# Performance work log

Measured on AMD Instinct MI355X. Metric: run time of the kernel, lower is better.

Reference implementation:

```python
import jax, jax.numpy as jnp
import numpy as np

H = 256
H2 = H // 2
N = 1024
T = 12
B = 4


def setup_inputs() -> dict:
    key = jax.random.key(0)
    ks = jax.random.split(key, 12)
    s = lambda fan_in: 1.0 / np.sqrt(fan_in)
    inp = {
        "node_embeddings": jax.random.normal(ks[0], (B, N, H), jnp.float32),
        # origin encoder: Linear(H,H) -> ReLU -> Linear(H,H2)
        "W1o": jax.random.normal(ks[1], (H, H), jnp.float32) * s(H),
        "b1o": jnp.zeros((H,), jnp.float32),
        "W2o": jax.random.normal(ks[2], (H, H2), jnp.float32) * s(H),
        "b2o": jnp.zeros((H2,), jnp.float32),
        # dest encoder
        "W1d": jax.random.normal(ks[3], (H, H), jnp.float32) * s(H),
        "b1d": jnp.zeros((H,), jnp.float32),
        "W2d": jax.random.normal(ks[4], (H, H2), jnp.float32) * s(H),
        "b2d": jnp.zeros((H2,), jnp.float32),
        # bilinear: out = o @ Wb @ d^T + bb  (torch nn.Bilinear(H2,H2,1))
        "Wb": jax.random.normal(ks[5], (H2, H2), jnp.float32) * s(H2),
        "bb": jnp.zeros((), jnp.float32),
        # horizon predictor: Linear(1, T) -> ReLU
        "wh": jax.random.normal(ks[6], (T,), jnp.float32),
        "bh": jnp.zeros((T,), jnp.float32),
    }
    return inp


def reference(node_embeddings, W1o, b1o, W2o, b2o, W1d, b1d, W2d, b2d, Wb, bb, wh, bh):
    # encoders (dropout is identity at eval)
    o = jax.nn.relu(node_embeddings @ W1o + b1o) @ W2o + b2o      # (B,N,H2)
    d = jax.nn.relu(node_embeddings @ W1d + b1d) @ W2d + b2d      # (B,N,H2)
    # bilinear score without materializing (B,N,N,H2):
    oW = jnp.einsum("bik,kl->bil", o, Wb)                          # (B,N,H2)
    scores = jnp.einsum("bil,bjl->bij", oW, d) + bb                # (B,N,N)
    # horizon predictor Linear(1,T)+ReLU, then permute to (B,T,N,N)
    pred = jax.nn.relu(scores[..., None] * wh + bh)                # (B,N,N,T)
    pred = jnp.transpose(pred, (0, 3, 1, 2))                       # (B,T,N,N)
    return jax.nn.relu(pred)
```

## Files before the change

kernel.cpp:

```cpp
#include <hip/hip_runtime.h>
#include <hip/hip_bf16.h>

constexpr int H  = 256;
constexpr int H2 = 128;
constexpr int N  = 1024;
constexpr int T  = 12;
constexpr int B  = 4;
constexpr int M  = B * N;

using short8 = __attribute__((ext_vector_type(8))) short;
using f32x4  = __attribute__((ext_vector_type(4))) float;

__device__ __forceinline__ unsigned short f2bf(float f) {
    union { float f; unsigned int u; } v; v.f = f;
    unsigned int u = v.u;
    u += 0x7FFFu + ((u >> 16) & 1u);
    return (unsigned short)(u >> 16);
}

__global__ void fold_wb_kernel(const float* __restrict__ W2o,
                               const float* __restrict__ b2o,
                               const float* __restrict__ Wb,
                               float* __restrict__ W2of,
                               float* __restrict__ b2of) {
    __shared__ float row[H2];
    const int i = blockIdx.x;
    const int j = threadIdx.x;
    const float* src = (i < H) ? (W2o + i * H2) : b2o;
    row[j] = src[j];
    __syncthreads();
    float acc = 0.f;
#pragma unroll 8
    for (int k = 0; k < H2; ++k) acc = fmaf(row[k], Wb[k * H2 + j], acc);
    if (i < H) W2of[i * H2 + j] = acc;
    else       b2of[j] = acc;
}

__global__ void prep_kernel(const float* __restrict__ x,
                            const float* __restrict__ W1o, const float* __restrict__ W1d,
                            const float* __restrict__ b1o, const float* __restrict__ b1d,
                            const float* __restrict__ W2of, const float* __restrict__ b2of,
                            const float* __restrict__ W2d,  const float* __restrict__ b2d,
                            unsigned short* __restrict__ xb,
                            unsigned short* __restrict__ W1T,
                            unsigned short* __restrict__ W2T,
                            float* __restrict__ bias1, float* __restrict__ bias2)
{
    const int NX  = M * H;
    const int NW1 = 512 * H;
    const int NW2 = 256 * H;
    const int TOT = NX + NW1 + NW2 + 512 + 256;
    for (int i = blockIdx.x * blockDim.x + threadIdx.x; i < TOT;
         i += gridDim.x * blockDim.x) {
        if (i < NX) {
            xb[i] = f2bf(x[i]);
        } else if (i < NX + NW1) {
            const int j = i - NX, n = j >> 8, k = j & 255;
            const float v = (n < 256) ? W1o[k * H + n] : W1d[k * H + (n - 256)];
            W1T[j] = f2bf(v);
        } else if (i < NX + NW1 + NW2) {
            const int j = i - NX - NW1, n = j >> 8, k = j & 255;
            const float v = (n < 128) ? W2of[k * H2 + n] : W2d[k * H2 + (n - 128)];
            W2T[j] = f2bf(v);
        } else if (i < NX + NW1 + NW2 + 512) {
            const int j = i - NX - NW1 - NW2;
            bias1[j] = (j < 256) ? b1o[j] : b1d[j - 256];
        } else {
            const int j = i - NX - NW1 - NW2 - 512;
            bias2[j] = (j < 128) ? b2of[j] : b2d[j - 128];
        }
    }
}

template<bool RELU>
__device__ __forceinline__ void enc_body(
    const unsigned short* __restrict__ A, int lda,
    const unsigned short* __restrict__ Bt,
    const float* __restrict__ bias,
    unsigned short* __restrict__ C, int ldc)
{
    __shared__ unsigned short Abuf[64 * 40];
    __shared__ unsigned short Bbuf[64 * 40];
    const int tid = threadIdx.x;
    const int w  = tid >> 6;
    const int l  = tid & 63;
    const int lr = tid >> 2;
    const int lk = (tid & 3) * 8;

    uint4 aR = *(const uint4*)(A + (size_t)lr * lda + lk);
    uint4 bR = *(const uint4*)(Bt + (size_t)lr * 256 + lk);

    f32x4 z = {0.f, 0.f, 0.f, 0.f};
    f32x4 acc[4] = {z, z, z, z};

    for (int kc = 0; kc < 256; kc += 32) {
        if (kc) __syncthreads();
        *(uint4*)&Abuf[lr * 40 + lk] = aR;
        *(uint4*)&Bbuf[lr * 40 + lk] = bR;
        __syncthreads();
        if (kc + 32 < 256) {
            aR = *(const uint4*)(A + (size_t)lr * lda + kc + 32 + lk);
            bR = *(const uint4*)(Bt + (size_t)lr * 256 + kc + 32 + lk);
        }
        const int q8 = (l >> 4) * 8;
        const short8 bf = *(const short8*)&Bbuf[(w * 16 + (l & 15)) * 40 + q8];
#pragma unroll
        for (int it = 0; it < 4; ++it) {
            const short8 af = *(const short8*)&Abuf[(it * 16 + (l & 15)) * 40 + q8];
            acc[it] = __builtin_amdgcn_mfma_f32_16x16x32_bf16(af, bf, acc[it], 0, 0, 0);
        }
    }

    const int n  = w * 16 + (l & 15);
    const int r0 = (l >> 4) * 4;
    const float bn = bias[n];
#pragma unroll
    for (int it = 0; it < 4; ++it)
#pragma unroll
        for (int r = 0; r < 4; ++r) {
            float v = acc[it][r] + bn;
            if (RELU) v = fmaxf(v, 0.f);
            C[(size_t)(it * 16 + r0 + r) * ldc + n] = f2bf(v);
        }
}

__global__ __launch_bounds__(256) void enc1_kernel(
    const unsigned short* __restrict__ xb, const unsigned short* __restrict__ W1T,
    const float* __restrict__ bias1, unsigned short* __restrict__ h)
{
    const int bx = blockIdx.x, by = blockIdx.y;
    enc_body<true>(xb + (size_t)by * 64 * 256, 256,
                   W1T + (size_t)bx * 64 * 256,
                   bias1 + bx * 64,
                   h + (size_t)by * 64 * 512 + bx * 64, 512);
}

__global__ __launch_bounds__(256) void enc2_kernel(
    const unsigned short* __restrict__ h, const unsigned short* __restrict__ W2T,
    const float* __restrict__ bias2, unsigned short* __restrict__ od)
{
    const int bx = blockIdx.x, by = blockIdx.y;
    enc_body<false>(h + (size_t)by * 64 * 512 + (bx >> 1) * 256, 512,
                    W2T + (size_t)bx * 64 * 256,
                    bias2 + bx * 64,
                    od + (size_t)by * 64 * 256 + bx * 64, 256);
}

__global__ __launch_bounds__(256) void k3_kernel(
    const unsigned short* __restrict__ od,
    const float* __restrict__ bbp, const float* __restrict__ wh,
    const float* __restrict__ bh, float* __restrict__ out)
{
    __shared__ unsigned short Abuf[64 * 40];
    __shared__ unsigned short Bbuf[64 * 40];
    const int tid = threadIdx.x;
    const int w  = tid >> 6;
    const int l  = tid & 63;
    const int lr = tid >> 2;
    const int lk = (tid & 3) * 8;
    const int b  = blockIdx.z;
    const int i0 = blockIdx.y * 64;
    const int j0 = blockIdx.x * 64;
    const unsigned short* Ab = od + ((size_t)b * N + i0) * 256;
    const unsigned short* Bb = od + ((size_t)b * N + j0) * 256 + 128;

    uint4 aR = *(const uint4*)(Ab + (size_t)lr * 256 + lk);
    uint4 bR = *(const uint4*)(Bb + (size_t)lr * 256 + lk);

    f32x4 z = {0.f, 0.f, 0.f, 0.f};
    f32x4 acc[4] = {z, z, z, z};

    for (int kc = 0; kc < H2; kc += 32) {
        if (kc) __syncthreads();
        *(uint4*)&Abuf[lr * 40 + lk] = aR;
        *(uint4*)&Bbuf[lr * 40 + lk] = bR;
        __syncthreads();
        if (kc + 32 < H2) {
            aR = *(const uint4*)(Ab + (size_t)lr * 256 + kc + 32 + lk);
            bR = *(const uint4*)(Bb + (size_t)lr * 256 + kc + 32 + lk);
        }
        const int q8 = (l >> 4) * 8;
        const short8 bf = *(const short8*)&Bbuf[(w * 16 + (l & 15)) * 40 + q8];
#pragma unroll
        for (int it = 0; it < 4; ++it) {
            const short8 af = *(const short8*)&Abuf[(it * 16 + (l & 15)) * 40 + q8];
            acc[it] = __builtin_amdgcn_mfma_f32_16x16x32_bf16(af, bf, acc[it], 0, 0, 0);
        }
    }

    const float bbv = bbp[0];
    float s[4][4];
#pragma unroll
    for (int it = 0; it < 4; ++it)
#pragma unroll
        for (int r = 0; r < 4; ++r) s[it][r] = acc[it][r] + bbv;

    const int jcol = j0 + w * 16 + (l & 15);
    const int r0   = (l >> 4) * 4;
#pragma unroll
    for (int t = 0; t < T; ++t) {
        const float wt = wh[t], bt = bh[t];
        float* ob = out + ((size_t)(b * T + t) * N + i0 + r0) * N + jcol;
#pragma unroll
        for (int it = 0; it < 4; ++it)
#pragma unroll
            for (int r = 0; r < 4; ++r)
                ob[(size_t)(it * 16 + r) * N] = fmaxf(fmaf(s[it][r], wt, bt), 0.f);
    }
}

extern "C" void kernel_launch(void* const* d_in, const int* in_sizes, int n_in,
                              void* d_out, int out_size, void* d_ws, size_t ws_size,
                              hipStream_t stream) {
    const float* x   = (const float*)d_in[0];
    const float* W1o = (const float*)d_in[1];
    const float* b1o = (const float*)d_in[2];
    const float* W2o = (const float*)d_in[3];
    const float* b2o = (const float*)d_in[4];
    const float* W1d = (const float*)d_in[5];
    const float* b1d = (const float*)d_in[6];
    const float* W2d = (const float*)d_in[7];
    const float* b2d = (const float*)d_in[8];
    const float* Wb  = (const float*)d_in[9];
    const float* bb  = (const float*)d_in[10];
    const float* wh  = (const float*)d_in[11];
    const float* bh  = (const float*)d_in[12];
    float* out = (float*)d_out;

    float* W2of  = (float*)d_ws;
    float* b2of  = W2of + H * H2;
    float* bias1 = b2of + H2;
    float* bias2 = bias1 + 512;
    unsigned short* xb  = (unsigned short*)(bias2 + 256);
    unsigned short* W1T = xb + (size_t)M * H;
    unsigned short* W2T = W1T + 512 * H;
    unsigned short* h   = W2T + 256 * H;
    unsigned short* od  = h + (size_t)M * 512;

    fold_wb_kernel<<<H + 1, H2, 0, stream>>>(W2o, b2o, Wb, W2of, b2of);

    prep_kernel<<<1024, 256, 0, stream>>>(x, W1o, W1d, b1o, b1d,
                                          W2of, b2of, W2d, b2d,
                                          xb, W1T, W2T, bias1, bias2);

    enc1_kernel<<<dim3(8, M / 64), 256, 0, stream>>>(xb, W1T, bias1, h);

    enc2_kernel<<<dim3(4, M / 64), 256, 0, stream>>>(h, W2T, bias2, od);

    k3_kernel<<<dim3(N / 64, N / 64, B), 256, 0, stream>>>(od, bb, wh, bh, out);
}
```

Baseline: 250.5 us.

## Fuse Wb fold into prep kernel and write score outputs as float4 rows

Drops the separate fold_wb kernel by computing the W2o·Wb product inline in prep_kernel, removing one launch. The k3 kernel swaps the MFMA operand roles so each lane holds four consecutive j columns of one i row. The epilogue can then issue 16-byte vector stores along the contiguous output dimension instead of scalar strided stores. The cost is a redundant 128-length dot product per W2T element in prep, done by fewer threads.

```diff
diff --git a/kernel.cpp b/kernel.cpp
--- a/kernel.cpp
+++ b/kernel.cpp
@@ -18,29 +18,12 @@
     return (unsigned short)(u >> 16);
 }
 
-__global__ void fold_wb_kernel(const float* __restrict__ W2o,
-                               const float* __restrict__ b2o,
-                               const float* __restrict__ Wb,
-                               float* __restrict__ W2of,
-                               float* __restrict__ b2of) {
-    __shared__ float row[H2];
-    const int i = blockIdx.x;
-    const int j = threadIdx.x;
-    const float* src = (i < H) ? (W2o + i * H2) : b2o;
-    row[j] = src[j];
-    __syncthreads();
-    float acc = 0.f;
-#pragma unroll 8
-    for (int k = 0; k < H2; ++k) acc = fmaf(row[k], Wb[k * H2 + j], acc);
-    if (i < H) W2of[i * H2 + j] = acc;
-    else       b2of[j] = acc;
-}
-
 __global__ void prep_kernel(const float* __restrict__ x,
                             const float* __restrict__ W1o, const float* __restrict__ W1d,
                             const float* __restrict__ b1o, const float* __restrict__ b1d,
-                            const float* __restrict__ W2of, const float* __restrict__ b2of,
-                            const float* __restrict__ W2d,  const float* __restrict__ b2d,
+                            const float* __restrict__ W2o, const float* __restrict__ b2o,
+                            const float* __restrict__ W2d, const float* __restrict__ b2d,
+                            const float* __restrict__ Wb,
                             unsigned short* __restrict__ xb,
                             unsigned short* __restrict__ W1T,
                             unsigned short* __restrict__ W2T,
@@ -60,14 +43,33 @@
             W1T[j] = f2bf(v);
         } else if (i < NX + NW1 + NW2) {
             const int j = i - NX - NW1, n = j >> 8, k = j & 255;
-            const float v = (n < 128) ? W2of[k * H2 + n] : W2d[k * H2 + (n - 128)];
+            float v;
+            if (n < 128) {
+                float acc = 0.f;
+#pragma unroll 8
+                for (int l2 = 0; l2 < H2; ++l2)
+                    acc = fmaf(W2o[k * H2 + l2], Wb[l2 * H2 + n], acc);
+                v = acc;
+            } else {
+                v = W2d[k * H2 + (n - 128)];
+            }
             W2T[j] = f2bf(v);
         } else if (i < NX + NW1 + NW2 + 512) {
             const int j = i - NX - NW1 - NW2;
             bias1[j] = (j < 256) ? b1o[j] : b1d[j - 256];
         } else {
             const int j = i - NX - NW1 - NW2 - 512;
-            bias2[j] = (j < 128) ? b2of[j] : b2d[j - 128];
+            float v;
+            if (j < 128) {
+                float acc = 0.f;
+#pragma unroll 8
+                for (int l2 = 0; l2 < H2; ++l2)
+                    acc = fmaf(b2o[l2], Wb[l2 * H2 + j], acc);
+                v = acc;
+            } else {
+                v = b2d[j - 128];
+            }
+            bias2[j] = v;
         }
     }
 }
@@ -151,8 +153,8 @@
     const float* __restrict__ bbp, const float* __restrict__ wh,
     const float* __restrict__ bh, float* __restrict__ out)
 {
-    __shared__ unsigned short Abuf[64 * 40];
-    __shared__ unsigned short Bbuf[64 * 40];
+    __shared__ unsigned short Obuf[64 * 40];
+    __shared__ unsigned short Dbuf[64 * 40];
     const int tid = threadIdx.x;
     const int w  = tid >> 6;
     const int l  = tid & 63;
@@ -161,29 +163,29 @@
     const int b  = blockIdx.z;
     const int i0 = blockIdx.y * 64;
     const int j0 = blockIdx.x * 64;
-    const unsigned short* Ab = od + ((size_t)b * N + i0) * 256;
-    const unsigned short* Bb = od + ((size_t)b * N + j0) * 256 + 128;
-
-    uint4 aR = *(const uint4*)(Ab + (size_t)lr * 256 + lk);
-    uint4 bR = *(const uint4*)(Bb + (size_t)lr * 256 + lk);
+    const unsigned short* Ob = od + ((size_t)b * N + i0) * 256;
+    const unsigned short* Db = od + ((size_t)b * N + j0) * 256 + 128;
+
+    uint4 oR = *(const uint4*)(Ob + (size_t)lr * 256 + lk);
+    uint4 dR = *(const uint4*)(Db + (size_t)lr * 256 + lk);
 
     f32x4 z = {0.f, 0.f, 0.f, 0.f};
     f32x4 acc[4] = {z, z, z, z};
 
     for (int kc = 0; kc < H2; kc += 32) {
         if (kc) __syncthreads();
-        *(uint4*)&Abuf[lr * 40 + lk] = aR;
-        *(uint4*)&Bbuf[lr * 40 + lk] = bR;
+        *(uint4*)&Obuf[lr * 40 + lk] = oR;
+        *(uint4*)&Dbuf[lr * 40 + lk] = dR;
         __syncthreads();
         if (kc + 32 < H2) {
-            aR = *(const uint4*)(Ab + (size_t)lr * 256 + kc + 32 + lk);
-            bR = *(const uint4*)(Bb + (size_t)lr * 256 + kc + 32 + lk);
+            oR = *(const uint4*)(Ob + (size_t)lr * 256 + kc + 32 + lk);
+            dR = *(const uint4*)(Db + (size_t)lr * 256 + kc + 32 + lk);
         }
         const int q8 = (l >> 4) * 8;
-        const short8 bf = *(const short8*)&Bbuf[(w * 16 + (l & 15)) * 40 + q8];
+        const short8 bf = *(const short8*)&Obuf[(w * 16 + (l & 15)) * 40 + q8];
 #pragma unroll
         for (int it = 0; it < 4; ++it) {
-            const short8 af = *(const short8*)&Abuf[(it * 16 + (l & 15)) * 40 + q8];
+            const short8 af = *(const short8*)&Dbuf[(it * 16 + (l & 15)) * 40 + q8];
             acc[it] = __builtin_amdgcn_mfma_f32_16x16x32_bf16(af, bf, acc[it], 0, 0, 0);
         }
     }
@@ -195,17 +197,20 @@
 #pragma unroll
         for (int r = 0; r < 4; ++r) s[it][r] = acc[it][r] + bbv;
 
-    const int jcol = j0 + w * 16 + (l & 15);
+    const int iRow = i0 + w * 16 + (l & 15);
     const int r0   = (l >> 4) * 4;
 #pragma unroll
     for (int t = 0; t < T; ++t) {
         const float wt = wh[t], bt = bh[t];
-        float* ob = out + ((size_t)(b * T + t) * N + i0 + r0) * N + jcol;
-#pragma unroll
-        for (int it = 0; it < 4; ++it)
+        float* ob = out + ((size_t)(b * T + t) * N + iRow) * N + j0 + r0;
+#pragma unroll
+        for (int it = 0; it < 4; ++it) {
+            f32x4 v;
 #pragma unroll
             for (int r = 0; r < 4; ++r)
-                ob[(size_t)(it * 16 + r) * N] = fmaxf(fmaf(s[it][r], wt, bt), 0.f);
+                v[r] = fmaxf(fmaf(s[it][r], wt, bt), 0.f);
+            *(f32x4*)(ob + it * 16) = v;
+        }
     }
 }
 
@@ -227,9 +232,7 @@
     const float* bh  = (const float*)d_in[12];
     float* out = (float*)d_out;
 
-    float* W2of  = (float*)d_ws;
-    float* b2of  = W2of + H * H2;
-    float* bias1 = b2of + H2;
+    float* bias1 = (float*)d_ws;
     float* bias2 = bias1 + 512;
     unsigned short* xb  = (unsigned short*)(bias2 + 256);
     unsigned short* W1T = xb + (size_t)M * H;
@@ -237,10 +240,8 @@
     unsigned short* h   = W2T + 256 * H;
     unsigned short* od  = h + (size_t)M * 512;
 
-    fold_wb_kernel<<<H + 1, H2, 0, stream>>>(W2o, b2o, Wb, W2of, b2of);
-
     prep_kernel<<<1024, 256, 0, stream>>>(x, W1o, W1d, b1o, b1d,
-                                          W2of, b2of, W2d, b2d,
+                                          W2o, b2o, W2d, b2d, Wb,
                                           xb, W1T, W2T, bias1, bias2);
 
     enc1_kernel<<<dim3(8, M / 64), 256, 0, stream>>>(xb, W1T, bias1, h);
```

Measured after the change: 248.9 us. Within noise of the previous version (-0.7%).
